# Optimization experiments

Measured on AMD Instinct MI355X. Metric: run time of the kernel, lower is better.

The kernel has to match this reference:

```python
import jax, jax.numpy as jnp
import numpy as np
from jax import lax

NUM_HEADS = 8
EPS = 1e-12  # torch F.normalize eps


def setup_inputs() -> dict:
    key = jax.random.key(0)
    ks = jax.random.split(key, 5)
    dim = 192
    b, h, w = 8, 128, 128
    return {
        "x": jax.random.normal(ks[0], (b, dim, h, w), jnp.float32),
        "w_qkv": jax.random.normal(ks[1], (3 * dim, dim, 1, 1), jnp.float32) * (1.0 / np.sqrt(dim)),
        "w_dw": jax.random.normal(ks[2], (3 * dim, 1, 3, 3), jnp.float32) * (1.0 / 3.0),
        "w_proj": jax.random.normal(ks[3], (dim, dim, 1, 1), jnp.float32) * (1.0 / np.sqrt(dim)),
        "temperature": jnp.ones((NUM_HEADS, 1, 1), jnp.float32),
    }


def _l2norm(t):
    n = jnp.sqrt(jnp.sum(t * t, axis=-1, keepdims=True))
    return t / jnp.maximum(n, EPS)


def reference(x, w_qkv, w_dw, w_proj, temperature):
    b, c, h, w = x.shape
    # 1x1 conv to 3*dim channels
    qkv = jnp.einsum('bchw,oc->bohw', x, w_qkv[:, :, 0, 0])
    # depthwise 3x3 conv, dilation=2, padding=2, groups=3*dim
    qkv = lax.conv_general_dilated(
        qkv, w_dw, window_strides=(1, 1), padding=((2, 2), (2, 2)),
        rhs_dilation=(2, 2), feature_group_count=3 * c,
        dimension_numbers=('NCHW', 'OIHW', 'NCHW'))
    q, k, v = jnp.split(qkv, 3, axis=1)
    ch = c // NUM_HEADS
    def heads(t):  # b (head ch) h w -> b head ch (h w)
        return t.reshape(b, NUM_HEADS, ch, h * w)
    q, k, v = heads(q), heads(k), heads(v)
    q = _l2norm(q)
    k = _l2norm(k)
    attn = jnp.einsum('bhcn,bhdn->bhcd', q, k) * temperature  # (b, head, ch, ch)
    attn = jax.nn.softmax(attn, axis=-1)
    out = jnp.einsum('bhcd,bhdn->bhcn', attn, v)
    out = out.reshape(b, c, h, w)
    out = jnp.einsum('bchw,oc->bohw', out, w_proj[:, :, 0, 0])
    return out
```

## Files before the change

### kernel.cpp

```cpp
#include <hip/hip_runtime.h>


#define DIM 192
#define NH 8
#define CH 24
#define IH 128
#define IW 128
#define NPIX (IH*IW)
#define BATCH 8
#define QKVC (3*DIM)
#define PAD 200
#define SPAD 264

typedef unsigned short u16;
typedef short bf16x8 __attribute__((ext_vector_type(8)));
typedef float f32x4 __attribute__((ext_vector_type(4)));

__device__ __forceinline__ float b2f(u16 u){
    unsigned v = ((unsigned)u) << 16;
    return __builtin_bit_cast(float, v);
}
__device__ __forceinline__ u16 f2b(float f){
    unsigned u = __builtin_bit_cast(unsigned, f);
    u += 0x7fffu + ((u >> 16) & 1u);
    return (u16)(u >> 16);
}

__device__ __forceinline__ void conv_row8(const u16* __restrict__ rp, int px0,
        float w0, float w1, float w2, float* o_){
    float f[12];
    if(px0 > 0){
        unsigned u = *(const unsigned*)(rp + px0 - 2);
        f[0] = b2f((u16)u); f[1] = b2f((u16)(u >> 16));
    } else { f[0] = 0.f; f[1] = 0.f; }
    bf16x8 v = *(const bf16x8*)(rp + px0);
    #pragma unroll
    for(int j=0;j<8;j++) f[2+j] = b2f((u16)v[j]);
    if(px0 < 120){
        unsigned u = *(const unsigned*)(rp + px0 + 8);
        f[10] = b2f((u16)u); f[11] = b2f((u16)(u >> 16));
    } else { f[10] = 0.f; f[11] = 0.f; }
    #pragma unroll
    for(int i=0;i<8;i++) o_[i] += w0*f[i] + w1*f[i+2] + w2*f[i+4];
}

__global__ __launch_bounds__(256) void k0_wcvt(const float* __restrict__ wqkv,
        u16* __restrict__ wb){
    int i = (blockIdx.x*256 + threadIdx.x)*4;
    f32x4 v = *(const f32x4*)&wqkv[i];
    unsigned lo = ((unsigned)f2b(v[1]) << 16) | f2b(v[0]);
    unsigned hi = ((unsigned)f2b(v[3]) << 16) | f2b(v[2]);
    *(uint2*)&wb[i] = make_uint2(lo, hi);
}

__global__ __launch_bounds__(256) void k1_qkv(const float* __restrict__ x,
        const u16* __restrict__ wb, u16* __restrict__ qkv_pre){
    __shared__ __align__(16) u16 Xl[64*PAD];
    const int tid = threadIdx.x;
    const int pt = blockIdx.x, b = blockIdx.y;
    const int p0 = pt*64;
    {
        const int px = tid & 63, grp = tid >> 6;
        const float* xb = x + (size_t)b*DIM*NPIX + p0 + px;
        #pragma unroll
        for(int cg = 0; cg < 6; cg++){
            int cb = grp*48 + cg*8;
            bf16x8 v;
            #pragma unroll
            for(int j=0;j<8;j++) v[j] = (short)f2b(xb[(size_t)(cb+j)*NPIX]);
            *(bf16x8*)&Xl[px*PAD + cb] = v;
        }
    }
    __syncthreads();
    const int lane = tid & 63, w = tid >> 6;
    const int r = lane & 15, quad = lane >> 4;
    u16* op = qkv_pre + (size_t)b*QKVC*NPIX + p0;
    for(int i = 0; i < 9; i++){
        const int ob = (w*9 + i)*16;
        f32x4 acc[4];
        { f32x4 z = {0.f,0.f,0.f,0.f}; for(int j=0;j<4;j++) acc[j]=z; }
        const u16* wp = wb + (size_t)(ob + r)*DIM;
        #pragma unroll
        for(int kk = 0; kk < 6; kk++){
            const int k0 = kk*32 + quad*8;
            bf16x8 a0 = *(const bf16x8*)&wp[k0];
            #pragma unroll
            for(int ni=0; ni<4; ni++){
                bf16x8 bb = *(const bf16x8*)&Xl[(ni*16 + r)*PAD + k0];
                acc[ni] = __builtin_amdgcn_mfma_f32_16x16x32_bf16(bb, a0, acc[ni], 0,0,0);
            }
        }
        #pragma unroll
        for(int ni=0; ni<4; ni++){
            int o = ob + r;
            int px = ni*16 + quad*4;
            f32x4 a = acc[ni];
            unsigned lo = ((unsigned)f2b(a[1]) << 16) | f2b(a[0]);
            unsigned hi = ((unsigned)f2b(a[3]) << 16) | f2b(a[2]);
            *(uint2*)&op[(size_t)o*NPIX + px] = make_uint2(lo, hi);
        }
    }
}

__global__ __launch_bounds__(256) void k2_gram(const u16* __restrict__ qkv_pre,
        const float* __restrict__ wdw, float* __restrict__ G){
    __shared__ __align__(16) u16 Sl[48*SPAD];
    const int tid = threadIdx.x;
    const int pc = blockIdx.x, h = blockIdx.y, b = blockIdx.z;
    const int lane = tid & 63, w = tid >> 6;
    const int r = lane & 15, quad = lane >> 4;
    f32x4 acc[6];
    { f32x4 z = {0.f,0.f,0.f,0.f}; for(int i=0;i<6;i++) acc[i]=z; }
    for(int chunk = 0; chunk < 2; chunk++){
        if(chunk) __syncthreads();
        for(int it = 0; it < 6; it++){
            int t = tid + it*256;
            int c48 = t >> 5, oct = t & 31;
            int isK = (c48 >= CH);
            int c = isK ? (c48 - CH) : c48;
            int ch = (isK ? DIM : 0) + h*CH + c;
            const u16* base = qkv_pre + ((size_t)b*QKVC + ch)*NPIX;
            const float* wv = wdw + ch*9;
            int py = pc*4 + chunk*2 + (oct >> 4);
            int px0 = (oct & 15)*8;
            float o_[8];
            #pragma unroll
            for(int i=0;i<8;i++) o_[i]=0.f;
            #pragma unroll
            for(int ky=0;ky<3;ky++){
                int ry = py + 2*ky - 2;
                if(ry < 0 || ry >= IH) continue;
                conv_row8(base + ry*IW, px0, wv[ky*3], wv[ky*3+1], wv[ky*3+2], o_);
            }
            bf16x8 v;
            #pragma unroll
            for(int i=0;i<8;i++) v[i] = (short)f2b(o_[i]);
            *(bf16x8*)&Sl[c48*SPAD + oct*8] = v;
        }
        __syncthreads();
        #pragma unroll
        for(int kk = 0; kk < 2; kk++){
            const int k0 = w*64 + kk*32 + quad*8;
            bf16x8 f0 = *(const bf16x8*)&Sl[(     r)*SPAD + k0];
            bf16x8 f1 = *(const bf16x8*)&Sl[(16 + r)*SPAD + k0];
            bf16x8 f2 = *(const bf16x8*)&Sl[(32 + r)*SPAD + k0];
            acc[0] = __builtin_amdgcn_mfma_f32_16x16x32_bf16(f0, f0, acc[0], 0,0,0);
            acc[1] = __builtin_amdgcn_mfma_f32_16x16x32_bf16(f0, f1, acc[1], 0,0,0);
            acc[2] = __builtin_amdgcn_mfma_f32_16x16x32_bf16(f0, f2, acc[2], 0,0,0);
            acc[3] = __builtin_amdgcn_mfma_f32_16x16x32_bf16(f1, f1, acc[3], 0,0,0);
            acc[4] = __builtin_amdgcn_mfma_f32_16x16x32_bf16(f1, f2, acc[4], 0,0,0);
            acc[5] = __builtin_amdgcn_mfma_f32_16x16x32_bf16(f2, f2, acc[5], 0,0,0);
        }
    }
    __syncthreads();
    float* R = (float*)Sl;
    #pragma unroll
    for(int tile=0; tile<6; tile++)
        *(f32x4*)&R[(w*6 + tile)*256 + lane*4] = acc[tile];
    __syncthreads();
    float* Gb = G + (size_t)(b*NH + h)*48*48;
    #pragma unroll
    for(int i=0; i<6; i++){
        int idx = tid + i*256;
        int tile = idx >> 8, rem = idx & 255;
        int ln = rem >> 2, t = rem & 3;
        float s = R[idx] + R[1536 + idx] + R[2*1536 + idx] + R[3*1536 + idx];
        int ti = (tile<3) ? 0 : ((tile<5) ? 1 : 2);
        int tj = (tile<3) ? tile : ((tile<5) ? (tile-2) : 2);
        int c = ti*16 + (ln >> 4)*4 + t;
        int d = tj*16 + (ln & 15);
        atomicAdd(&Gb[c*48 + d], s);
    }
}

__global__ __launch_bounds__(256) void k4_vconv(u16* __restrict__ qkv_pre,
        const float* __restrict__ wdw){
    const int tid = threadIdx.x;
    const int oct = tid & 15, pyl = tid >> 4;
    const int band = blockIdx.x, cp = blockIdx.y, b = blockIdx.z;
    const int py = band*16 + pyl, px0 = oct*8;
    #pragma unroll
    for(int j=0;j<2;j++){
        int ch = cp*2 + j;
        const u16* base = qkv_pre + ((size_t)b*QKVC + 2*DIM + ch)*NPIX;
        const float* wv = wdw + (2*DIM + ch)*9;
        float o_[8];
        #pragma unroll
        for(int i=0;i<8;i++) o_[i]=0.f;
        #pragma unroll
        for(int ky=0;ky<3;ky++){
            int ry = py + 2*ky - 2;
            if(ry < 0 || ry >= IH) continue;
            conv_row8(base + ry*IW, px0, wv[ky*3], wv[ky*3+1], wv[ky*3+2], o_);
        }
        bf16x8 v;
        #pragma unroll
        for(int i=0;i<8;i++) v[i] = (short)f2b(o_[i]);
        *(bf16x8*)&qkv_pre[((size_t)b*QKVC + ch)*NPIX + py*IW + px0] = v;
    }
}

__global__ __launch_bounds__(256) void k3_attn(const float* __restrict__ G,
        const float* __restrict__ temp, const float* __restrict__ wproj,
        u16* __restrict__ M){
    __shared__ float attn[NH][CH][CH];
    __shared__ float nq[DIM], nk[DIM];
    const int b = blockIdx.x, tid = threadIdx.x;
    const float* Gb = G + (size_t)b*NH*48*48;
    if(tid < DIM){
        int h = tid / CH, c = tid % CH;
        const float* g = Gb + (size_t)h*48*48;
        nq[tid] = fmaxf(sqrtf(g[c*48 + c]), 1e-12f);
        nk[tid] = fmaxf(sqrtf(g[(CH+c)*48 + (CH+c)]), 1e-12f);
    }
    __syncthreads();
    if(tid < DIM){
        int h = tid / CH, c = tid % CH;
        float t = temp[h];
        const float* g = Gb + (size_t)h*48*48 + c*48 + CH;
        float row[CH];
        float mx = -1e30f;
        #pragma unroll
        for(int d=0; d<CH; d++){
            float v = g[d] / (nq[tid]*nk[h*CH+d]) * t;
            row[d]=v; mx = fmaxf(mx,v);
        }
        float sum=0.f;
        #pragma unroll
        for(int d=0;d<CH;d++){ row[d]=expf(row[d]-mx); sum+=row[d]; }
        float inv = 1.f/sum;
        #pragma unroll
        for(int d=0;d<CH;d++) attn[h][c][d] = row[d]*inv;
    }
    __syncthreads();
    u16* Mb = M + (size_t)b*DIM*DIM;
    for(int i = tid; i < DIM*DIM; i += 256){
        int o = i / DIM, hd = i % DIM;
        int h = hd / CH, d = hd % CH;
        float s = 0.f;
        #pragma unroll
        for(int c=0;c<CH;c++)
            s += wproj[o*DIM + h*CH + c] * attn[h][c][d];
        Mb[i] = f2b(s);
    }
}

__global__ __launch_bounds__(256) void k5_out(const u16* __restrict__ qkv_pre,
        const u16* __restrict__ M, float* __restrict__ out){
    __shared__ __align__(16) u16 vl[64*PAD];
    const int tid = threadIdx.x;
    const int pt = blockIdx.x, b = blockIdx.y;
    const int p0 = pt*64;
    {
        const int px = tid & 63, grp = tid >> 6;
        const u16* vb = qkv_pre + (size_t)b*QKVC*NPIX + p0 + px;
        #pragma unroll
        for(int cg = 0; cg < 6; cg++){
            int cb = grp*48 + cg*8;
            bf16x8 v;
            #pragma unroll
            for(int j=0;j<8;j++) v[j] = (short)vb[(size_t)(cb+j)*NPIX];
            *(bf16x8*)&vl[px*PAD + cb] = v;
        }
    }
    __syncthreads();
    const int lane = tid & 63, w = tid >> 6;
    const int r = lane & 15, quad = lane >> 4;
    const u16* Mb = M + (size_t)b*DIM*DIM;
    float* op = out + (size_t)b*DIM*NPIX + p0;
    for(int i = 0; i < 3; i++){
        const int ob = (w*3 + i)*16;
        f32x4 acc[4];
        { f32x4 z = {0.f,0.f,0.f,0.f}; for(int j=0;j<4;j++) acc[j]=z; }
        const u16* mp = Mb + (size_t)(ob + r)*DIM;
        #pragma unroll
        for(int kk = 0; kk < 6; kk++){
            const int k0 = kk*32 + quad*8;
            bf16x8 a0 = *(const bf16x8*)&mp[k0];
            #pragma unroll
            for(int ni=0; ni<4; ni++){
                bf16x8 bb = *(const bf16x8*)&vl[(ni*16 + r)*PAD + k0];
                acc[ni] = __builtin_amdgcn_mfma_f32_16x16x32_bf16(bb, a0, acc[ni], 0,0,0);
            }
        }
        #pragma unroll
        for(int ni=0; ni<4; ni++)
            *(f32x4*)&op[(size_t)(ob + r)*NPIX + ni*16 + quad*4] = acc[ni];
    }
}

extern "C" void kernel_launch(void* const* d_in, const int* in_sizes, int n_in,
                              void* d_out, int out_size, void* d_ws, size_t ws_size,
                              hipStream_t stream){
    const float* x     = (const float*)d_in[0];
    const float* wqkv  = (const float*)d_in[1];
    const float* wdw   = (const float*)d_in[2];
    const float* wproj = (const float*)d_in[3];
    const float* temp  = (const float*)d_in[4];
    float* out = (float*)d_out;

    char* ws = (char*)d_ws;
    u16* qkv_pre = (u16*)ws;
    size_t off = (size_t)BATCH*QKVC*NPIX*sizeof(u16);
    float* G  = (float*)(ws + off); off += (size_t)BATCH*NH*48*48*4;
    u16* M    = (u16*)(ws + off);   off += (size_t)BATCH*DIM*DIM*2;
    u16* wb   = (u16*)(ws + off);   off += (size_t)QKVC*DIM*2;

    hipMemsetAsync(G, 0, (size_t)BATCH*NH*48*48*sizeof(float), stream);

    k0_wcvt<<<108, 256, 0, stream>>>(wqkv, wb);
    k1_qkv <<<dim3(256, BATCH), 256, 0, stream>>>(x, wb, qkv_pre);
    k2_gram<<<dim3(32, NH, BATCH), 256, 0, stream>>>(qkv_pre, wdw, G);
    k4_vconv<<<dim3(8, 96, BATCH), 256, 0, stream>>>(qkv_pre, wdw);
    k3_attn<<<BATCH, 256, 0, stream>>>(G, temp, wproj, M);
    k5_out <<<dim3(256, BATCH), 256, 0, stream>>>(qkv_pre, M, out);
}
```

Measured before the change: 435.0 us.

## Fuse V depthwise conv into output projection kernel

Removes the separate V depthwise-conv kernel that wrote convolved V back into global memory. The output kernel now computes the dilated 3x3 conv for its own row of 64 pixels directly from the pre-conv V and stores the transposed result into LDS for the MFMA projection. This avoids one full write and one strided read of V through global memory, plus a kernel launch. In exchange, each block recomputes its conv rows and does scattered 32-bit LDS stores, which can cause bank conflicts.

```diff
diff --git a/kernel.cpp b/kernel.cpp
--- a/kernel.cpp
+++ b/kernel.cpp
@@ -173,33 +173,6 @@
     }
 }
 
-__global__ __launch_bounds__(256) void k4_vconv(u16* __restrict__ qkv_pre,
-        const float* __restrict__ wdw){
-    const int tid = threadIdx.x;
-    const int oct = tid & 15, pyl = tid >> 4;
-    const int band = blockIdx.x, cp = blockIdx.y, b = blockIdx.z;
-    const int py = band*16 + pyl, px0 = oct*8;
-    #pragma unroll
-    for(int j=0;j<2;j++){
-        int ch = cp*2 + j;
-        const u16* base = qkv_pre + ((size_t)b*QKVC + 2*DIM + ch)*NPIX;
-        const float* wv = wdw + (2*DIM + ch)*9;
-        float o_[8];
-        #pragma unroll
-        for(int i=0;i<8;i++) o_[i]=0.f;
-        #pragma unroll
-        for(int ky=0;ky<3;ky++){
-            int ry = py + 2*ky - 2;
-            if(ry < 0 || ry >= IH) continue;
-            conv_row8(base + ry*IW, px0, wv[ky*3], wv[ky*3+1], wv[ky*3+2], o_);
-        }
-        bf16x8 v;
-        #pragma unroll
-        for(int i=0;i<8;i++) v[i] = (short)f2b(o_[i]);
-        *(bf16x8*)&qkv_pre[((size_t)b*QKVC + ch)*NPIX + py*IW + px0] = v;
-    }
-}
-
 __global__ __launch_bounds__(256) void k3_attn(const float* __restrict__ G,
         const float* __restrict__ temp, const float* __restrict__ wproj,
         u16* __restrict__ M){
@@ -245,22 +218,36 @@
     }
 }
 
-__global__ __launch_bounds__(256) void k5_out(const u16* __restrict__ qkv_pre,
-        const u16* __restrict__ M, float* __restrict__ out){
-    __shared__ __align__(16) u16 vl[64*PAD];
+__global__ __launch_bounds__(256) void k45_out(const u16* __restrict__ qkv_pre,
+        const float* __restrict__ wdw, const u16* __restrict__ M,
+        float* __restrict__ out){
+    __shared__ __align__(16) u16 Vt[64*PAD];
     const int tid = threadIdx.x;
-    const int pt = blockIdx.x, b = blockIdx.y;
-    const int p0 = pt*64;
-    {
-        const int px = tid & 63, grp = tid >> 6;
-        const u16* vb = qkv_pre + (size_t)b*QKVC*NPIX + p0 + px;
-        #pragma unroll
-        for(int cg = 0; cg < 6; cg++){
-            int cb = grp*48 + cg*8;
-            bf16x8 v;
-            #pragma unroll
-            for(int j=0;j<8;j++) v[j] = (short)vb[(size_t)(cb+j)*NPIX];
-            *(bf16x8*)&vl[px*PAD + cb] = v;
+    const int half = blockIdx.x & 1, py = blockIdx.x >> 1, b = blockIdx.y;
+    const int p0 = py*IW + half*64;
+    for(int it = 0; it < 3; it++){
+        int t = tid + it*256;
+        int chp = t >> 3, oct = t & 7;
+        int px0g = half*64 + oct*8;
+        float oo[2][8];
+        #pragma unroll
+        for(int j=0;j<2;j++){
+            int ch = 2*chp + j;
+            const u16* base = qkv_pre + ((size_t)b*QKVC + 2*DIM + ch)*NPIX;
+            const float* wv = wdw + (2*DIM + ch)*9;
+            #pragma unroll
+            for(int i=0;i<8;i++) oo[j][i]=0.f;
+            #pragma unroll
+            for(int ky=0;ky<3;ky++){
+                int ry = py + 2*ky - 2;
+                if(ry < 0 || ry >= IH) continue;
+                conv_row8(base + ry*IW, px0g, wv[ky*3], wv[ky*3+1], wv[ky*3+2], oo[j]);
+            }
+        }
+        #pragma unroll
+        for(int i=0;i<8;i++){
+            unsigned pk = (unsigned)f2b(oo[0][i]) | ((unsigned)f2b(oo[1][i]) << 16);
+            *(unsigned*)&Vt[(oct*8+i)*PAD + 2*chp] = pk;
         }
     }
     __syncthreads();
@@ -279,7 +266,7 @@
             bf16x8 a0 = *(const bf16x8*)&mp[k0];
             #pragma unroll
             for(int ni=0; ni<4; ni++){
-                bf16x8 bb = *(const bf16x8*)&vl[(ni*16 + r)*PAD + k0];
+                bf16x8 bb = *(const bf16x8*)&Vt[(ni*16 + r)*PAD + k0];
                 acc[ni] = __builtin_amdgcn_mfma_f32_16x16x32_bf16(bb, a0, acc[ni], 0,0,0);
             }
         }
@@ -311,7 +298,6 @@
     k0_wcvt<<<108, 256, 0, stream>>>(wqkv, wb);
     k1_qkv <<<dim3(256, BATCH), 256, 0, stream>>>(x, wb, qkv_pre);
     k2_gram<<<dim3(32, NH, BATCH), 256, 0, stream>>>(qkv_pre, wdw, G);
-    k4_vconv<<<dim3(8, 96, BATCH), 256, 0, stream>>>(qkv_pre, wdw);
     k3_attn<<<BATCH, 256, 0, stream>>>(G, temp, wproj, M);
-    k5_out <<<dim3(256, BATCH), 256, 0, stream>>>(qkv_pre, M, out);
-}
+    k45_out<<<dim3(256, BATCH), 256, 0, stream>>>(qkv_pre, wdw, M, out);
+}
```

Result: slower. 446.6 us (+2.7%).
